# Kernel tuning notes

Measured on AMD Instinct MI355X. Metric: run time of the kernel, lower is better.

## Reference

```python
import jax, jax.numpy as jnp
import numpy as np

N = 50000       # nodes
E_RAND = 800000 # random edges (avg degree ~16)
K = 64          # edges touching `node`; setup_inputs guarantees exactly K
F = 64          # num_node_features
C = 64          # conv_channels


def setup_inputs() -> dict:
    key = jax.random.key(0)
    ks = jax.random.split(key, 6)
    x = jax.random.normal(ks[0], (N, F), dtype=jnp.float32)
    # random edges avoiding node 0 so exactly the K prepended edges touch node 0
    src = jax.random.randint(ks[1], (E_RAND,), 1, N, dtype=jnp.int64)
    dst = jax.random.randint(ks[2], (E_RAND,), 1, N, dtype=jnp.int64)
    ksrc = jnp.zeros((K,), dtype=jnp.int64)
    kdst = jnp.arange(1, K + 1, dtype=jnp.int64)
    edge_index = jnp.stack([jnp.concatenate([ksrc, src]),
                            jnp.concatenate([kdst, dst])])  # [2, K+E_RAND]
    W1 = jax.random.normal(ks[3], (F, C), jnp.float32) / np.float32(np.sqrt(F))
    b1 = jnp.zeros((C,), jnp.float32)
    W2 = jax.random.normal(ks[4], (C, C), jnp.float32) / np.float32(np.sqrt(C))
    b2 = jnp.zeros((C,), jnp.float32)
    Wr = jax.random.normal(ks[5], (C, 1), jnp.float32) / np.float32(np.sqrt(C))
    br = jnp.zeros((1,), jnp.float32)
    return {"x": x, "edge_index": edge_index, "node": 0,
            "W1": W1, "b1": b1, "W2": W2, "b2": b2, "Wr": Wr, "br": br}


def gcn_conv(x, src, dst, W, b):
    """PyG GCNConv with self-loops already appended to (src, dst).
    out[v] = sum_{(u,v)} deg(u)^-1/2 * deg(v)^-1/2 * (x @ W)[u] + b
    """
    n = x.shape[0]
    xw = x @ W                                              # [N, C]
    deg = jnp.zeros((n,), xw.dtype).at[dst].add(1.0)        # in-degree incl. self-loop
    dinv = jnp.where(deg > 0, jax.lax.rsqrt(deg), 0.0)
    norm = dinv[src] * dinv[dst]                            # [E]
    out = jax.ops.segment_sum(xw[src] * norm[:, None], dst, num_segments=n)
    return out + b


def reference(x, edge_index, node, W1, b1, W2, b2, Wr, br):
    n = x.shape[0]
    loop = jnp.arange(n, dtype=edge_index.dtype)
    src = jnp.concatenate([edge_index[0], loop])  # add self loops (GCNConv default)
    dst = jnp.concatenate([edge_index[1], loop])
    h = jax.nn.relu(gcn_conv(x, src, dst, W1, b1))
    h = jax.nn.relu(gcn_conv(h, src, dst, W2, b2))
    # edges incident to `node` (setup guarantees exactly K such edges)
    s0, d0 = edge_index[0], edge_index[1]
    mask = (s0 == node) | (d0 == node)
    idx = jnp.nonzero(mask, size=K)[0]
    s, d = s0[idx], d0[idx]
    targets = jnp.where(s == node, d, s)  # self-loop (s==d==node) -> node
    score = h[targets] @ Wr + br          # [K, 1]
    score = jax.nn.softmax(score, axis=0)
    return score[:, 0], targets
```

## Files before the change

### kernel.cpp

```cpp
#include <hip/hip_runtime.h>
#include <math.h>

#define KK 64
#define CAP 64
#define NF 4160

__global__ __launch_bounds__(256) void k_find(const int* __restrict__ ei, int E,
                                              const int* __restrict__ nodep,
                                              int4* __restrict__ zbase, int zcount4,
                                              float* __restrict__ h1s,
                                              int* __restrict__ tcount,
                                              int* __restrict__ tpairs) {
    int idx = blockIdx.x * 256 + threadIdx.x;
    if (idx < zcount4) zbase[idx] = make_int4(0, 0, 0, 0);
    if (idx < 64) h1s[(size_t)NF * 64 + idx] = 0.f;
    int node = nodep[0];
    int n4 = E >> 2;
    if (idx < n4) {
        int4 ss = ((const int4*)ei)[idx];
        int4 dd = ((const int4*)(ei + E))[idx];
        int s[4] = {ss.x, ss.y, ss.z, ss.w};
        int d[4] = {dd.x, dd.y, dd.z, dd.w};
#pragma unroll
        for (int k = 0; k < 4; k++) {
            if (s[k] == node || d[k] == node) {
                int q = atomicAdd(tcount, 1);
                if (q < KK) { int e = idx * 4 + k; tpairs[2 * q] = e; tpairs[2 * q + 1] = (s[k] == node) ? d[k] : s[k]; }
            }
        }
    }
    if (idx == 0) {
        for (int e = n4 * 4; e < E; e++) {
            int s = ei[e], d = ei[E + e];
            if (s == node || d == node) {
                int q = atomicAdd(tcount, 1);
                if (q < KK) { tpairs[2 * q] = e; tpairs[2 * q + 1] = (s == node) ? d : s; }
            }
        }
    }
}

__global__ void k_tsort(const int* __restrict__ tpairs, int* __restrict__ tsorted,
                        int* __restrict__ towner, int* __restrict__ tflag) {
    __shared__ int eidx[KK], tgt[KK], srt[KK];
    int t = threadIdx.x;
    eidx[t] = tpairs[2 * t];
    tgt[t] = tpairs[2 * t + 1];
    __syncthreads();
    int rank = 0;
    for (int j = 0; j < KK; j++) rank += (eidx[j] < eidx[t]) ? 1 : 0;
    srt[rank] = tgt[t];
    __syncthreads();
    int mynode = srt[t];
    int owner = t;
    for (int j = 0; j < t; j++) if (srt[j] == mynode) { owner = j; break; }
    tsorted[t] = mynode;
    towner[t] = owner;
    if (owner == t) tflag[mynode] = t + 1;
}

__global__ __launch_bounds__(256) void k_cct(const int* __restrict__ ei, int E,
                                             const int* __restrict__ tflag,
                                             int* __restrict__ cnt,
                                             int* __restrict__ tcnt2,
                                             int* __restrict__ tslots) {
    int n4 = E >> 2;
    int e4 = blockIdx.x * 256 + threadIdx.x;
    if (e4 < n4) {
        int4 ss = ((const int4*)ei)[e4];
        int4 dd = ((const int4*)(ei + E))[e4];
        int s[4] = {ss.x, ss.y, ss.z, ss.w};
        int d[4] = {dd.x, dd.y, dd.z, dd.w};
#pragma unroll
        for (int k = 0; k < 4; k++) {
            atomicAdd(&cnt[d[k]], 1);
            int f = tflag[d[k]];
            if (f) { int p = atomicAdd(&tcnt2[f - 1], 1); if (p < CAP) tslots[(f - 1) * CAP + p] = s[k]; }
        }
    }
    if (blockIdx.x == 0 && threadIdx.x == 0) {
        for (int e = n4 * 4; e < E; e++) {
            int d = ei[E + e];
            atomicAdd(&cnt[d], 1);
            int f = tflag[d];
            if (f) { int p = atomicAdd(&tcnt2[f - 1], 1); if (p < CAP) tslots[(f - 1) * CAP + p] = ei[e]; }
        }
    }
}

__global__ __launch_bounds__(1024) void k_fbuild(const int* __restrict__ tsorted,
                                                 const int* __restrict__ towner,
                                                 const int* __restrict__ tcnt2,
                                                 const int* __restrict__ tslots,
                                                 int* __restrict__ fnode,
                                                 int* __restrict__ fmapRow,
                                                 int* __restrict__ fidx) {
    int tid = threadIdx.x;
    for (int i = tid; i < NF; i += 1024) {
        int tp = i / 65, j = i % 65;
        int own = towner[tp];
        int u;
        if (j == 0) u = tsorted[tp];
        else {
            int c = tcnt2[own]; if (c > CAP) c = CAP;
            u = (j - 1 < c) ? tslots[own * CAP + (j - 1)] : -1;
        }
        fnode[i] = u;
    }
    __syncthreads();
    for (int i = tid; i < NF; i += 1024) {
        int u = fnode[i];
        if (u >= 0) atomicCAS(&fmapRow[u], 0, i + 1);
    }
    __syncthreads();
    for (int i = tid; i < NF; i += 1024) {
        int u = fnode[i];
        fidx[i] = (u >= 0) ? (fmapRow[u] - 1) : NF;
    }
}

__global__ __launch_bounds__(256) void k_collect_f(const int* __restrict__ ei, int E,
                                                   const int* __restrict__ fmapRow,
                                                   int* __restrict__ fcnt,
                                                   int* __restrict__ fslots) {
    int n4 = E >> 2;
    int e4 = blockIdx.x * 256 + threadIdx.x;
    if (e4 < n4) {
        int4 ss = ((const int4*)ei)[e4];
        int4 dd = ((const int4*)(ei + E))[e4];
        int s[4] = {ss.x, ss.y, ss.z, ss.w};
        int d[4] = {dd.x, dd.y, dd.z, dd.w};
#pragma unroll
        for (int k = 0; k < 4; k++) {
            int r = fmapRow[d[k]];
            if (r) { int p = atomicAdd(&fcnt[r - 1], 1); if (p < CAP) fslots[(size_t)(r - 1) * CAP + p] = s[k]; }
        }
    }
    if (blockIdx.x == 0 && threadIdx.x == 0) {
        for (int e = n4 * 4; e < E; e++) {
            int r = fmapRow[ei[E + e]];
            if (r) { int p = atomicAdd(&fcnt[r - 1], 1); if (p < CAP) fslots[(size_t)(r - 1) * CAP + p] = ei[e]; }
        }
    }
}

__global__ __launch_bounds__(256) void k_layer1(const float* __restrict__ x,
                                                const int* __restrict__ fnode,
                                                const int* __restrict__ fmapRow,
                                                const int* __restrict__ cnt,
                                                const int* __restrict__ fcnt,
                                                const int* __restrict__ fslots,
                                                const float* __restrict__ W1,
                                                const float* __restrict__ b1,
                                                float* __restrict__ h1s) {
    __shared__ __align__(16) float W1s[64 * 64];
    int tid = threadIdx.x;
    for (int i = tid; i < 1024; i += 256) ((float4*)W1s)[i] = ((const float4*)W1)[i];
    __syncthreads();
    int i = blockIdx.x * 4 + (tid >> 6);
    int lane = tid & 63;
    if (i >= NF) return;
    int u = fnode[i];
    if (u < 0 || fmapRow[u] != i + 1) return;
    float du = rsqrtf((float)(cnt[u] + 1));
    float acc = du * x[(size_t)u * 64 + lane];
    int c = fcnt[i]; if (c > CAP) c = CAP;
    const int* sl = fslots + (size_t)i * CAP;
    int k = 0;
    for (; k + 4 <= c; k += 4) {
        int u0 = sl[k], u1 = sl[k + 1], u2 = sl[k + 2], u3 = sl[k + 3];
        float f0 = rsqrtf((float)(cnt[u0] + 1));
        float f1 = rsqrtf((float)(cnt[u1] + 1));
        float f2 = rsqrtf((float)(cnt[u2] + 1));
        float f3 = rsqrtf((float)(cnt[u3] + 1));
        acc += f0 * x[(size_t)u0 * 64 + lane] + f1 * x[(size_t)u1 * 64 + lane]
             + f2 * x[(size_t)u2 * 64 + lane] + f3 * x[(size_t)u3 * 64 + lane];
    }
    for (; k < c; k++) {
        int uu = sl[k];
        acc += rsqrtf((float)(cnt[uu] + 1)) * x[(size_t)uu * 64 + lane];
    }
    float z = du * acc;
    float h = 0.f;
#pragma unroll
    for (int f = 0; f < 64; f++) h += __shfl(z, f) * W1s[f * 64 + lane];
    h = fmaxf(h + b1[lane], 0.f);
    h1s[(size_t)i * 64 + lane] = du * h;
}

__global__ __launch_bounds__(64) void k_score2(const float* __restrict__ h1s,
                                               const int* __restrict__ fidx,
                                               const int* __restrict__ tsorted,
                                               const int* __restrict__ cnt,
                                               const float* __restrict__ W2,
                                               const float* __restrict__ b2,
                                               const float* __restrict__ Wr,
                                               float* __restrict__ sc) {
    int tp = blockIdx.x;
    int lane = threadIdx.x;
    int t = tsorted[tp];
    float dt = rsqrtf((float)(cnt[t] + 1));
    const int* fx = fidx + tp * 65;
    float z = 0.f;
#pragma unroll
    for (int j = 0; j < 65; j++) {
        int idx = fx[j];
        z += h1s[(size_t)idx * 64 + lane];
    }
    z *= dt;
    float acc = 0.f;
#pragma unroll
    for (int f = 0; f < 64; f++) acc += __shfl(z, f) * W2[f * 64 + lane];
    float h2 = fmaxf(acc + b2[lane], 0.f);
    float p = h2 * Wr[lane];
#pragma unroll
    for (int off = 32; off >= 1; off >>= 1) p += __shfl_xor(p, off);
    if (lane == 0) sc[tp] = p;
}

__global__ void k_softmax(const float* __restrict__ sc, const int* __restrict__ tsorted,
                          float* __restrict__ out) {
    int t = threadIdx.x;
    float s = sc[t];
    float m = s;
#pragma unroll
    for (int off = 32; off >= 1; off >>= 1) m = fmaxf(m, __shfl_xor(m, off));
    float e = __expf(s - m);
    float ss = e;
#pragma unroll
    for (int off = 32; off >= 1; off >>= 1) ss += __shfl_xor(ss, off);
    out[t] = e / ss;
    out[KK + t] = (float)tsorted[t];
}

extern "C" void kernel_launch(void* const* d_in, const int* in_sizes, int n_in,
                              void* d_out, int out_size, void* d_ws, size_t ws_size,
                              hipStream_t stream) {
    const float* x  = (const float*)d_in[0];
    const int*   ei = (const int*)d_in[1];
    const int*   nodep = (const int*)d_in[2];
    const float* W1 = (const float*)d_in[3];
    const float* b1 = (const float*)d_in[4];
    const float* W2 = (const float*)d_in[5];
    const float* b2 = (const float*)d_in[6];
    const float* Wr = (const float*)d_in[7];
    const float* br = (const float*)d_in[8];
    float* out = (float*)d_out;
    (void)br;

    int N = in_sizes[0] / 64;
    int E = in_sizes[1] / 2;

    char* w = (char*)d_ws;
    int* cnt     = (int*)w; w += (size_t)N * 4;
    int* tflag   = (int*)w; w += (size_t)N * 4;
    int* fmapRow = (int*)w; w += (size_t)N * 4;
    int* fcnt    = (int*)w; w += (size_t)NF * 4;
    int* tcnt2   = (int*)w; w += KK * 4;
    int zcount4 = (3 * N + NF + KK) / 4;
    int* tcount  = (int*)w; w += 16;
    int* tpairs  = (int*)w; w += 2 * KK * 4;
    int* tsorted = (int*)w; w += KK * 4;
    int* towner  = (int*)w; w += KK * 4;
    int* fnode   = (int*)w; w += (size_t)NF * 4;
    int* fidx    = (int*)w; w += (size_t)NF * 4;
    int* tslots  = (int*)w; w += (size_t)KK * CAP * 4;
    int* fslots  = (int*)w; w += (size_t)NF * CAP * 4;
    float* h1s   = (float*)w; w += (size_t)(NF + 1) * 64 * 4;
    float* sc    = (float*)w; w += KK * 4;

    hipMemsetAsync(tcount, 0, 16, stream);

    int ebl = (E / 4 + 255) / 256;
    k_find<<<ebl, 256, 0, stream>>>(ei, E, nodep, (int4*)cnt, zcount4, h1s, tcount, tpairs);
    k_tsort<<<1, 64, 0, stream>>>(tpairs, tsorted, towner, tflag);
    k_cct<<<ebl, 256, 0, stream>>>(ei, E, tflag, cnt, tcnt2, tslots);
    k_fbuild<<<1, 1024, 0, stream>>>(tsorted, towner, tcnt2, tslots, fnode, fmapRow, fidx);
    k_collect_f<<<ebl, 256, 0, stream>>>(ei, E, fmapRow, fcnt, fslots);
    k_layer1<<<(NF + 3) / 4, 256, 0, stream>>>(x, fnode, fmapRow, cnt, fcnt, fslots, W1, b1, h1s);
    k_score2<<<KK, 64, 0, stream>>>(h1s, fidx, tsorted, cnt, W2, b2, Wr, sc);
    k_softmax<<<1, 64, 0, stream>>>(sc, tsorted, out);
}
```

Measured before the change: 171.5 us.

## Fuse single-block stages into edge scans via last-block-done pattern; compact lookup tables

Folds the small single-block kernels (target sort, frontier build, softmax) into the tail of the preceding grid kernels, using an atomic done counter so that only the last block runs the serial step. Degree counting moves into the first edge scan, and zeroing is handled by one memset instead of a kernel store loop. The tflag and fmap lookup arrays shrink to 8-bit and 16-bit to cut random-access gather traffic. The aim is to remove launch gaps and memory traffic, at the cost of threadfence/atomic overhead and a serial tail on a single block.

```diff
diff --git a/kernel.cpp b/kernel.cpp
--- a/kernel.cpp
+++ b/kernel.cpp
@@ -5,14 +5,18 @@
 #define CAP 64
 #define NF 4160
 
-__global__ __launch_bounds__(256) void k_find(const int* __restrict__ ei, int E,
-                                              const int* __restrict__ nodep,
-                                              int4* __restrict__ zbase, int zcount4,
-                                              float* __restrict__ h1s,
-                                              int* __restrict__ tcount,
-                                              int* __restrict__ tpairs) {
-    int idx = blockIdx.x * 256 + threadIdx.x;
-    if (idx < zcount4) zbase[idx] = make_int4(0, 0, 0, 0);
+__global__ __launch_bounds__(256) void k_scan1(const int* __restrict__ ei, int E,
+                                               const int* __restrict__ nodep,
+                                               int* __restrict__ cnt,
+                                               int* __restrict__ tcount,
+                                               int* __restrict__ tpairs,
+                                               int* __restrict__ done,
+                                               int* __restrict__ tsorted,
+                                               int* __restrict__ towner,
+                                               unsigned char* __restrict__ tflag,
+                                               float* __restrict__ h1s) {
+    int tid = threadIdx.x;
+    int idx = blockIdx.x * 256 + tid;
     if (idx < 64) h1s[(size_t)NF * 64 + idx] = 0.f;
     int node = nodep[0];
     int n4 = E >> 2;
@@ -23,6 +27,7 @@
         int d[4] = {dd.x, dd.y, dd.z, dd.w};
 #pragma unroll
         for (int k = 0; k < 4; k++) {
+            atomicAdd(&cnt[d[k]], 1);
             if (s[k] == node || d[k] == node) {
                 int q = atomicAdd(tcount, 1);
                 if (q < KK) { int e = idx * 4 + k; tpairs[2 * q] = e; tpairs[2 * q + 1] = (s[k] == node) ? d[k] : s[k]; }
@@ -32,71 +37,76 @@
     if (idx == 0) {
         for (int e = n4 * 4; e < E; e++) {
             int s = ei[e], d = ei[E + e];
+            atomicAdd(&cnt[d], 1);
             if (s == node || d == node) {
                 int q = atomicAdd(tcount, 1);
                 if (q < KK) { tpairs[2 * q] = e; tpairs[2 * q + 1] = (s == node) ? d : s; }
             }
         }
     }
-}
-
-__global__ void k_tsort(const int* __restrict__ tpairs, int* __restrict__ tsorted,
-                        int* __restrict__ towner, int* __restrict__ tflag) {
+    __threadfence();
+    __shared__ int amLast;
+    if (tid == 0) amLast = (atomicAdd(done, 1) == (int)gridDim.x - 1);
+    __syncthreads();
+    if (!amLast) return;
+    __threadfence();
     __shared__ int eidx[KK], tgt[KK], srt[KK];
-    int t = threadIdx.x;
-    eidx[t] = tpairs[2 * t];
-    tgt[t] = tpairs[2 * t + 1];
-    __syncthreads();
-    int rank = 0;
-    for (int j = 0; j < KK; j++) rank += (eidx[j] < eidx[t]) ? 1 : 0;
-    srt[rank] = tgt[t];
-    __syncthreads();
-    int mynode = srt[t];
-    int owner = t;
-    for (int j = 0; j < t; j++) if (srt[j] == mynode) { owner = j; break; }
-    tsorted[t] = mynode;
-    towner[t] = owner;
-    if (owner == t) tflag[mynode] = t + 1;
-}
-
-__global__ __launch_bounds__(256) void k_cct(const int* __restrict__ ei, int E,
-                                             const int* __restrict__ tflag,
-                                             int* __restrict__ cnt,
-                                             int* __restrict__ tcnt2,
-                                             int* __restrict__ tslots) {
+    if (tid < KK) { eidx[tid] = tpairs[2 * tid]; tgt[tid] = tpairs[2 * tid + 1]; }
+    __syncthreads();
+    if (tid < KK) {
+        int rank = 0;
+        for (int j = 0; j < KK; j++) rank += (eidx[j] < eidx[tid]) ? 1 : 0;
+        srt[rank] = tgt[tid];
+    }
+    __syncthreads();
+    if (tid < KK) {
+        int mynode = srt[tid];
+        int owner = tid;
+        for (int j = 0; j < tid; j++) if (srt[j] == mynode) { owner = j; break; }
+        tsorted[tid] = mynode;
+        towner[tid] = owner;
+        if (owner == tid) tflag[mynode] = (unsigned char)(tid + 1);
+    }
+}
+
+__global__ __launch_bounds__(256) void k_scan2(const int* __restrict__ ei, int E,
+                                               const unsigned char* __restrict__ tflag,
+                                               int* __restrict__ tcnt2,
+                                               int* __restrict__ tslots,
+                                               int* __restrict__ done,
+                                               const int* __restrict__ tsorted,
+                                               const int* __restrict__ towner,
+                                               int* __restrict__ fnode,
+                                               int* __restrict__ fmapRow,
+                                               unsigned short* __restrict__ fmap16,
+                                               int* __restrict__ fidx) {
+    int tid = threadIdx.x;
+    int idx = blockIdx.x * 256 + tid;
     int n4 = E >> 2;
-    int e4 = blockIdx.x * 256 + threadIdx.x;
-    if (e4 < n4) {
-        int4 ss = ((const int4*)ei)[e4];
-        int4 dd = ((const int4*)(ei + E))[e4];
+    if (idx < n4) {
+        int4 ss = ((const int4*)ei)[idx];
+        int4 dd = ((const int4*)(ei + E))[idx];
         int s[4] = {ss.x, ss.y, ss.z, ss.w};
         int d[4] = {dd.x, dd.y, dd.z, dd.w};
 #pragma unroll
         for (int k = 0; k < 4; k++) {
-            atomicAdd(&cnt[d[k]], 1);
             int f = tflag[d[k]];
             if (f) { int p = atomicAdd(&tcnt2[f - 1], 1); if (p < CAP) tslots[(f - 1) * CAP + p] = s[k]; }
         }
     }
-    if (blockIdx.x == 0 && threadIdx.x == 0) {
+    if (idx == 0) {
         for (int e = n4 * 4; e < E; e++) {
-            int d = ei[E + e];
-            atomicAdd(&cnt[d], 1);
-            int f = tflag[d];
+            int f = tflag[ei[E + e]];
             if (f) { int p = atomicAdd(&tcnt2[f - 1], 1); if (p < CAP) tslots[(f - 1) * CAP + p] = ei[e]; }
         }
     }
-}
-
-__global__ __launch_bounds__(1024) void k_fbuild(const int* __restrict__ tsorted,
-                                                 const int* __restrict__ towner,
-                                                 const int* __restrict__ tcnt2,
-                                                 const int* __restrict__ tslots,
-                                                 int* __restrict__ fnode,
-                                                 int* __restrict__ fmapRow,
-                                                 int* __restrict__ fidx) {
-    int tid = threadIdx.x;
-    for (int i = tid; i < NF; i += 1024) {
+    __threadfence();
+    __shared__ int amLast;
+    if (tid == 0) amLast = (atomicAdd(done, 1) == (int)gridDim.x - 1);
+    __syncthreads();
+    if (!amLast) return;
+    __threadfence();
+    for (int i = tid; i < NF; i += 256) {
         int tp = i / 65, j = i % 65;
         int own = towner[tp];
         int u;
@@ -108,37 +118,43 @@
         fnode[i] = u;
     }
     __syncthreads();
-    for (int i = tid; i < NF; i += 1024) {
+    for (int i = tid; i < NF; i += 256) {
         int u = fnode[i];
         if (u >= 0) atomicCAS(&fmapRow[u], 0, i + 1);
     }
     __syncthreads();
-    for (int i = tid; i < NF; i += 1024) {
+    for (int i = tid; i < NF; i += 256) {
         int u = fnode[i];
-        fidx[i] = (u >= 0) ? (fmapRow[u] - 1) : NF;
-    }
-}
-
-__global__ __launch_bounds__(256) void k_collect_f(const int* __restrict__ ei, int E,
-                                                   const int* __restrict__ fmapRow,
-                                                   int* __restrict__ fcnt,
-                                                   int* __restrict__ fslots) {
+        if (u >= 0) {
+            int row = fmapRow[u];
+            fidx[i] = row - 1;
+            if (row == i + 1) fmap16[u] = (unsigned short)row;
+        } else {
+            fidx[i] = NF;
+        }
+    }
+}
+
+__global__ __launch_bounds__(256) void k_scan3(const int* __restrict__ ei, int E,
+                                               const unsigned short* __restrict__ fmap16,
+                                               int* __restrict__ fcnt,
+                                               int* __restrict__ fslots) {
+    int idx = blockIdx.x * 256 + threadIdx.x;
     int n4 = E >> 2;
-    int e4 = blockIdx.x * 256 + threadIdx.x;
-    if (e4 < n4) {
-        int4 ss = ((const int4*)ei)[e4];
-        int4 dd = ((const int4*)(ei + E))[e4];
+    if (idx < n4) {
+        int4 ss = ((const int4*)ei)[idx];
+        int4 dd = ((const int4*)(ei + E))[idx];
         int s[4] = {ss.x, ss.y, ss.z, ss.w};
         int d[4] = {dd.x, dd.y, dd.z, dd.w};
 #pragma unroll
         for (int k = 0; k < 4; k++) {
-            int r = fmapRow[d[k]];
+            int r = fmap16[d[k]];
             if (r) { int p = atomicAdd(&fcnt[r - 1], 1); if (p < CAP) fslots[(size_t)(r - 1) * CAP + p] = s[k]; }
         }
     }
-    if (blockIdx.x == 0 && threadIdx.x == 0) {
+    if (idx == 0 && blockIdx.x == 0) {
         for (int e = n4 * 4; e < E; e++) {
-            int r = fmapRow[ei[E + e]];
+            int r = fmap16[ei[E + e]];
             if (r) { int p = atomicAdd(&fcnt[r - 1], 1); if (p < CAP) fslots[(size_t)(r - 1) * CAP + p] = ei[e]; }
         }
     }
@@ -195,7 +211,9 @@
                                                const float* __restrict__ W2,
                                                const float* __restrict__ b2,
                                                const float* __restrict__ Wr,
-                                               float* __restrict__ sc) {
+                                               float* __restrict__ sc,
+                                               int* __restrict__ done,
+                                               float* __restrict__ out) {
     int tp = blockIdx.x;
     int lane = threadIdx.x;
     int t = tsorted[tp];
@@ -216,12 +234,13 @@
 #pragma unroll
     for (int off = 32; off >= 1; off >>= 1) p += __shfl_xor(p, off);
     if (lane == 0) sc[tp] = p;
-}
-
-__global__ void k_softmax(const float* __restrict__ sc, const int* __restrict__ tsorted,
-                          float* __restrict__ out) {
-    int t = threadIdx.x;
-    float s = sc[t];
+    __threadfence();
+    __shared__ int amLast;
+    if (lane == 0) amLast = (atomicAdd(done, 1) == (int)gridDim.x - 1);
+    __syncthreads();
+    if (!amLast) return;
+    __threadfence();
+    float s = sc[lane];
     float m = s;
 #pragma unroll
     for (int off = 32; off >= 1; off >>= 1) m = fmaxf(m, __shfl_xor(m, off));
@@ -229,8 +248,8 @@
     float ss = e;
 #pragma unroll
     for (int off = 32; off >= 1; off >>= 1) ss += __shfl_xor(ss, off);
-    out[t] = e / ss;
-    out[KK + t] = (float)tsorted[t];
+    out[lane] = e / ss;
+    out[KK + lane] = (float)tsorted[lane];
 }
 
 extern "C" void kernel_launch(void* const* d_in, const int* in_sizes, int n_in,
@@ -252,13 +271,19 @@
     int E = in_sizes[1] / 2;
 
     char* w = (char*)d_ws;
+    char* zstart = w;
     int* cnt     = (int*)w; w += (size_t)N * 4;
-    int* tflag   = (int*)w; w += (size_t)N * 4;
     int* fmapRow = (int*)w; w += (size_t)N * 4;
     int* fcnt    = (int*)w; w += (size_t)NF * 4;
     int* tcnt2   = (int*)w; w += KK * 4;
-    int zcount4 = (3 * N + NF + KK) / 4;
-    int* tcount  = (int*)w; w += 16;
+    int* tcount  = (int*)w; w += 4;
+    int* done1   = (int*)w; w += 4;
+    int* done2   = (int*)w; w += 4;
+    int* done3   = (int*)w; w += 4;
+    unsigned short* fmap16 = (unsigned short*)w; w += (size_t)N * 2;
+    unsigned char*  tflag  = (unsigned char*)w;  w += (size_t)N;
+    size_t zbytes = (size_t)(w - zstart);
+    w = zstart + ((zbytes + 15) & ~(size_t)15);
     int* tpairs  = (int*)w; w += 2 * KK * 4;
     int* tsorted = (int*)w; w += KK * 4;
     int* towner  = (int*)w; w += KK * 4;
@@ -269,15 +294,14 @@
     float* h1s   = (float*)w; w += (size_t)(NF + 1) * 64 * 4;
     float* sc    = (float*)w; w += KK * 4;
 
-    hipMemsetAsync(tcount, 0, 16, stream);
+    hipMemsetAsync(zstart, 0, zbytes, stream);
 
     int ebl = (E / 4 + 255) / 256;
-    k_find<<<ebl, 256, 0, stream>>>(ei, E, nodep, (int4*)cnt, zcount4, h1s, tcount, tpairs);
-    k_tsort<<<1, 64, 0, stream>>>(tpairs, tsorted, towner, tflag);
-    k_cct<<<ebl, 256, 0, stream>>>(ei, E, tflag, cnt, tcnt2, tslots);
-    k_fbuild<<<1, 1024, 0, stream>>>(tsorted, towner, tcnt2, tslots, fnode, fmapRow, fidx);
-    k_collect_f<<<ebl, 256, 0, stream>>>(ei, E, fmapRow, fcnt, fslots);
+    k_scan1<<<ebl, 256, 0, stream>>>(ei, E, nodep, cnt, tcount, tpairs, done1,
+                                     tsorted, towner, tflag, h1s);
+    k_scan2<<<ebl, 256, 0, stream>>>(ei, E, tflag, tcnt2, tslots, done2,
+                                     tsorted, towner, fnode, fmapRow, fmap16, fidx);
+    k_scan3<<<ebl, 256, 0, stream>>>(ei, E, fmap16, fcnt, fslots);
     k_layer1<<<(NF + 3) / 4, 256, 0, stream>>>(x, fnode, fmapRow, cnt, fcnt, fslots, W1, b1, h1s);
-    k_score2<<<KK, 64, 0, stream>>>(h1s, fidx, tsorted, cnt, W2, b2, Wr, sc);
-    k_softmax<<<1, 64, 0, stream>>>(sc, tsorted, out);
-}
+    k_score2<<<KK, 64, 0, stream>>>(h1s, fidx, tsorted, cnt, W2, b2, Wr, sc, done3, out);
+}
```

Measured after the change: 242.1 us. 1.41x slower.
